# Optimization experiments

Hardware: AMD Instinct MI355X
Metric: run time of the kernel (lower is better)

The kernel has to match this reference:

```python
import jax, jax.numpy as jnp
import numpy as np

B, S, DIM = 1, 2048, 4096
NH, NKV, HD = 32, 8, 128
REPEATS = NH // NKV
ROPE_THETA = 10000.0


def setup_inputs() -> dict:
    key = jax.random.key(0)
    ks = jax.random.split(key, 6)
    x = jax.random.normal(ks[0], (B, S, DIM), jnp.float32) * 0.02
    wq = jax.random.normal(ks[1], (NH * HD, DIM), jnp.float32) * 0.02
    wk = jax.random.normal(ks[2], (NKV * HD, DIM), jnp.float32) * 0.02
    wv = jax.random.normal(ks[3], (NKV * HD, DIM), jnp.float32) * 0.02
    wo = jax.random.normal(ks[4], (DIM, NH * HD), jnp.float32) * 0.02
    # rotary frequencies (real cos/sin form of complex freqs_cis)
    inv_freq = 1.0 / (ROPE_THETA ** (jnp.arange(0, HD, 2, dtype=jnp.float32) / HD))
    ang = jnp.arange(S, dtype=jnp.float32)[:, None] * inv_freq[None, :]  # [S, HD//2]
    freqs_cos = jnp.cos(ang)
    freqs_sin = jnp.sin(ang)
    positions = jnp.arange(S, dtype=jnp.int32)  # prompt phase: all positions
    # additive causal mask
    mask = jnp.where(jnp.tril(jnp.ones((S, S), bool)), 0.0, -1e9).astype(jnp.float32)
    cache_k = jnp.zeros((B, S, NKV, HD), jnp.float32)
    cache_v = jnp.zeros((B, S, NKV, HD), jnp.float32)
    return dict(x=x, wq=wq, wk=wk, wv=wv, wo=wo, freqs_cos=freqs_cos,
                freqs_sin=freqs_sin, cache_k=cache_k, cache_v=cache_v,
                positions=positions, mask=mask)


def apply_rope(t, cos, sin):
    # t: [b, s, h, d]; pairs are (d0,d1),(d2,d3),... matching view_as_complex
    tr = t[..., 0::2]
    ti = t[..., 1::2]
    c = cos[None, :, None, :]
    s = sin[None, :, None, :]
    out_r = tr * c - ti * s
    out_i = tr * s + ti * c
    return jnp.stack([out_r, out_i], axis=-1).reshape(t.shape)


def reference(x, wq, wk, wv, wo, freqs_cos, freqs_sin, cache_k, cache_v, positions, mask):
    b, s, _ = x.shape
    xq = jnp.einsum('bsd,od->bso', x, wq).reshape(b, s, NH, HD)
    xk = jnp.einsum('bsd,od->bso', x, wk).reshape(b, s, NKV, HD)
    xv = jnp.einsum('bsd,od->bso', x, wv).reshape(b, s, NKV, HD)
    xq = apply_rope(xq, freqs_cos, freqs_sin)
    xk = apply_rope(xk, freqs_cos, freqs_sin)
    # KV-cache scatter (prompt phase writes; output uses fresh xk/xv here)
    cache_k = cache_k.at[:, positions].set(xk)
    cache_v = cache_v.at[:, positions].set(xv)
    # GQA: repeat_interleave kv heads to match query heads
    k = jnp.repeat(xk, REPEATS, axis=2).transpose(0, 2, 1, 3)  # [b, NH, s, HD]
    v = jnp.repeat(xv, REPEATS, axis=2).transpose(0, 2, 1, 3)
    q = xq.transpose(0, 2, 1, 3)
    scale = HD ** -0.5
    scores = jnp.einsum('bhqd,bhkd->bhqk', q, k) * scale + mask[None, None]
    probs = jax.nn.softmax(scores.astype(jnp.float32), axis=-1).astype(q.dtype)
    out = jnp.einsum('bhqk,bhkd->bhqd', probs, v)
    out = out.transpose(0, 2, 1, 3).reshape(b, s, NH * HD)
    return jnp.einsum('bso,do->bsd', out, wo)
```

## Files before the change

kernel.cpp:

```cpp
#include <hip/hip_runtime.h>
#include <hip/hip_bf16.h>
#include <stdint.h>

typedef __bf16 bf16_t;
typedef __attribute__((ext_vector_type(8))) __bf16 bf16x8;
typedef __attribute__((ext_vector_type(4))) float f32x4;
typedef __attribute__((ext_vector_type(8))) unsigned short u16x8;

#define S_LEN 2048
#define DIM   4096
#define QKVN  6144
#define NHEAD 32
#define HDIM  128

typedef __attribute__((address_space(1))) unsigned int as1_u32;
typedef __attribute__((address_space(3))) unsigned int as3_u32;

__device__ __forceinline__ unsigned short f2bf(float f) {
  unsigned u = __builtin_bit_cast(unsigned, f);
  u += 0x7fffu + ((u >> 16) & 1u);
  return (unsigned short)(u >> 16);
}

__device__ __forceinline__ void gload_lds16(const void* g, void* l) {
  __builtin_amdgcn_global_load_lds(
      (as1_u32*)(unsigned long long)(uintptr_t)g,
      (as3_u32*)(unsigned int)(uintptr_t)l,
      16, 0, 0);
}

__global__ __launch_bounds__(256) void cvt5_kernel(const float* __restrict__ x,
                                                   const float* __restrict__ wq,
                                                   const float* __restrict__ wk,
                                                   const float* __restrict__ wv,
                                                   const float* __restrict__ wo,
                                                   ushort4* __restrict__ xb,
                                                   ushort4* __restrict__ wqkvb,
                                                   ushort4* __restrict__ wob) {
  const long N0 = 2097152;
  const long N1 = N0 + 4194304;
  const long N2 = N1 + 1048576;
  const long N3 = N2 + 1048576;
  const long N4 = N3 + 4194304;
  long idx = (long)blockIdx.x * 256 + threadIdx.x;
  long stride = (long)gridDim.x * 256;
  for (long i = idx; i < N4; i += stride) {
    const float4* s; ushort4* d; long o;
    if (i < N0)      { s = (const float4*)x;  d = xb;              o = i; }
    else if (i < N1) { s = (const float4*)wq; d = wqkvb;           o = i - N0; }
    else if (i < N2) { s = (const float4*)wk; d = wqkvb + 4194304; o = i - N1; }
    else if (i < N3) { s = (const float4*)wv; d = wqkvb + 5242880; o = i - N2; }
    else             { s = (const float4*)wo; d = wob;             o = i - N3; }
    float4 v = s[o];
    ushort4 r;
    r.x = f2bf(v.x); r.y = f2bf(v.y); r.z = f2bf(v.z); r.w = f2bf(v.w);
    d[o] = r;
  }
}

__device__ __forceinline__ void stage_A(const bf16_t* __restrict__ g, int ldk,
                                        long rowBase, int k0, char* ldsBase, int tid) {
#pragma unroll
  for (int i = 0; i < 2; ++i) {
    int c = tid + i * 512;
    int row = c >> 2, slot = c & 3;
    const bf16_t* src = g + (rowBase + row) * (long)ldk + k0
                        + ((slot ^ ((row >> 1) & 3)) << 3);
    gload_lds16(src, ldsBase + c * 16);
  }
}

__device__ __forceinline__ void stage_B(const bf16_t* __restrict__ g, int ldk,
                                        long rowBase, int k0, char* ldsBase, int tid) {
  int row = tid >> 2, slot = tid & 3;
  const bf16_t* src = g + (rowBase + row) * (long)ldk + k0
                      + ((slot ^ ((row >> 1) & 3)) << 3);
  gload_lds16(src, ldsBase + tid * 16);
}

__device__ __forceinline__ bf16x8 frag_ld(const char* base, int row, int lg) {
  return *(const bf16x8*)(base + row * 64 + ((lg ^ ((row >> 1) & 3)) << 4));
}

template <int OUTF32>
__global__ __launch_bounds__(512, 2) void gemm256(const bf16_t* __restrict__ A,
                                                  const bf16_t* __restrict__ B,
                                                  void* __restrict__ Cout,
                                                  int M, int N, int K, int nxt) {
  __shared__ char lds[49152];
  const int tid = threadIdx.x;
  const int lane = tid & 63, w = tid >> 6;
  const int wm = w >> 1, wn = w & 1;
  const int lg = lane >> 4, lr = lane & 15;
  const int nwg = gridDim.x;
  const int orig = blockIdx.x;
  const int wgid = (orig & 7) * (nwg >> 3) + (orig >> 3);
  const int bx = wgid % nxt, by = wgid / nxt;
  const long rowA = (long)by * 256;
  const long rowB = (long)bx * 128;

  f32x4 acc[4][4];
  const f32x4 z4 = {0.f, 0.f, 0.f, 0.f};
#pragma unroll
  for (int i = 0; i < 4; ++i)
#pragma unroll
    for (int j = 0; j < 4; ++j) acc[i][j] = z4;

  stage_A(A, K, rowA, 0, lds, tid);
  stage_B(B, K, rowB, 0, lds + 16384, tid);
  stage_A(A, K, rowA, 32, lds + 24576, tid);
  stage_B(B, K, rowB, 32, lds + 40960, tid);
  asm volatile("s_waitcnt vmcnt(3)" ::: "memory");
  __builtin_amdgcn_s_barrier();

  const int nt = K >> 5;
  for (int t = 0; t < nt; ++t) {
    char* Ab = lds + (t & 1) * 24576;
    char* Bb = Ab + 16384;
    bf16x8 af[4], bfr[4];
#pragma unroll
    for (int mf = 0; mf < 4; ++mf) af[mf] = frag_ld(Ab, wm * 64 + mf * 16 + lr, lg);
#pragma unroll
    for (int nf = 0; nf < 4; ++nf) bfr[nf] = frag_ld(Bb, wn * 64 + nf * 16 + lr, lg);
    asm volatile("s_waitcnt lgkmcnt(0)" ::: "memory");
    __builtin_amdgcn_sched_barrier(0);
    __builtin_amdgcn_s_barrier();
    if (t + 2 < nt) {
      stage_A(A, K, rowA, (t + 2) * 32, Ab, tid);
      stage_B(B, K, rowB, (t + 2) * 32, Bb, tid);
    }
    __builtin_amdgcn_s_setprio(1);
#pragma unroll
    for (int mf = 0; mf < 4; ++mf)
#pragma unroll
      for (int nf = 0; nf < 4; ++nf)
        acc[mf][nf] = __builtin_amdgcn_mfma_f32_16x16x32_bf16(af[mf], bfr[nf],
                                                              acc[mf][nf], 0, 0, 0);
    __builtin_amdgcn_s_setprio(0);
    if (t + 2 < nt) {
      asm volatile("s_waitcnt vmcnt(3)" ::: "memory");
    } else {
      asm volatile("s_waitcnt vmcnt(0)" ::: "memory");
    }
    __builtin_amdgcn_s_barrier();
  }

  const long crow = rowA + wm * 64;
  const long ccol = rowB + wn * 64;
  if (OUTF32) {
    float* C = (float*)Cout;
#pragma unroll
    for (int mf = 0; mf < 4; ++mf)
#pragma unroll
      for (int j = 0; j < 4; ++j) {
        long row = crow + mf * 16 + lg * 4 + j;
        float* cp = C + row * N + ccol + lr;
#pragma unroll
        for (int nf = 0; nf < 4; ++nf) cp[nf * 16] = acc[mf][nf][j];
      }
  } else {
    unsigned short* C = (unsigned short*)Cout;
#pragma unroll
    for (int mf = 0; mf < 4; ++mf)
#pragma unroll
      for (int j = 0; j < 4; ++j) {
        long row = crow + mf * 16 + lg * 4 + j;
        unsigned short* cp = C + row * N + ccol + lr;
#pragma unroll
        for (int nf = 0; nf < 4; ++nf) cp[nf * 16] = f2bf(acc[mf][nf][j]);
      }
  }
}

__global__ __launch_bounds__(256) void rope_kernel(unsigned int* __restrict__ qkv32,
                                                   const float* __restrict__ cosb,
                                                   const float* __restrict__ sinb) {
  int t = blockIdx.x * 256 + threadIdx.x;
  int i  = t & 63;
  int sh = t >> 6;
  int hh = sh % 40;
  int s  = sh / 40;
  int col2 = (hh < 32) ? (hh * 64 + i) : (2048 + (hh - 32) * 64 + i);
  unsigned int* p = qkv32 + (long)s * (QKVN / 2) + col2;
  unsigned int v = *p;
  float tr = __builtin_bit_cast(float, (v & 0xffffu) << 16);
  float ti = __builtin_bit_cast(float, v & 0xffff0000u);
  float c  = cosb[s * 64 + i];
  float sn = sinb[s * 64 + i];
  float orr = tr * c - ti * sn;
  float oi  = tr * sn + ti * c;
  *p = (unsigned int)f2bf(orr) | ((unsigned int)f2bf(oi) << 16);
}

__global__ __launch_bounds__(256) void vtrans_kernel(const bf16_t* __restrict__ qkv,
                                                     bf16_t* __restrict__ vT) {
  const int kh = blockIdx.x;
  const int hd = threadIdx.x & 127;
  const int s0 = blockIdx.y * 16 + (threadIdx.x >> 7) * 8;
  u16x8 v;
#pragma unroll
  for (int e = 0; e < 8; ++e)
    v[e] = *(const unsigned short*)(qkv + (long)(s0 + e) * QKVN + 5120 + kh * HDIM + hd);
  *(u16x8*)(vT + ((long)kh * HDIM + hd) * S_LEN + s0) = v;
}

__global__ __launch_bounds__(512) void attn_kernel(const bf16_t* __restrict__ qkv,
                                                   const bf16_t* __restrict__ vT,
                                                   unsigned short* __restrict__ ob) {
  __shared__ bf16_t Kt[64 * 128];
  __shared__ bf16_t Vt[128 * 64];
  __shared__ bf16_t Pl[8 * 16 * 64];
  const int h  = blockIdx.x;
  const int qi = 15 - (int)blockIdx.y;
  const int qb = qi * 128;
  const int kh = h >> 2;
  const int tid = threadIdx.x, lane = tid & 63, w = tid >> 6;
  const int lg = lane >> 4, lr = lane & 15;
  const int qrow0 = qb + w * 16;

  bf16x8 qf[4];
  const bf16_t* qptr = qkv + (long)(qrow0 + lr) * QKVN + h * HDIM + lg * 8;
#pragma unroll
  for (int kk = 0; kk < 4; ++kk) qf[kk] = *(const bf16x8*)(qptr + kk * 32);

  const f32x4 z4 = {0.f, 0.f, 0.f, 0.f};
  f32x4 oacc[8];
#pragma unroll
  for (int c = 0; c < 8; ++c) oacc[c] = z4;
  float m[4]    = {-1e30f, -1e30f, -1e30f, -1e30f};
  float lsum[4] = {0.f, 0.f, 0.f, 0.f};

  char* KtB = (char*)Kt;
  char* VtB = (char*)Vt;
  char* PlB = (char*)Pl + w * 2048;
  const float scale = 0.08838834764831845f;
  const int ntiles = 2 * qi + 2;
  const int wqmax = qrow0 + 15;

  for (int t = 0; t < ntiles; ++t) {
    const int kv0 = t * 64;
    __syncthreads();
#pragma unroll
    for (int it = 0; it < 2; ++it) {
      int cch = tid + it * 512;
      int r = cch >> 4, c = cch & 15;
      const bf16_t* src = qkv + (long)(kv0 + r) * QKVN + 4096 + kh * HDIM
                          + ((c ^ (r & 7)) * 8);
      gload_lds16(src, KtB + cch * 16);
    }
#pragma unroll
    for (int it = 0; it < 2; ++it) {
      int cch = tid + it * 512;
      int hd = cch >> 3, c = cch & 7;
      const bf16_t* src = vT + ((long)kh * HDIM + hd) * S_LEN + kv0
                          + ((c ^ (hd & 7)) * 8);
      gload_lds16(src, VtB + cch * 16);
    }
    __syncthreads();
    if (kv0 > wqmax) continue;

    f32x4 sf[4];
#pragma unroll
    for (int f = 0; f < 4; ++f) {
      f32x4 a = z4;
      int n = f * 16 + lr;
      int rb = n * 256, sw = (n & 7) << 4;
#pragma unroll
      for (int kk = 0; kk < 4; ++kk) {
        bf16x8 kf = *(const bf16x8*)(KtB + rb + (((kk * 4 + lg) * 16) ^ sw));
        a = __builtin_amdgcn_mfma_f32_16x16x32_bf16(qf[kk], kf, a, 0, 0, 0);
      }
      sf[f] = a;
    }

    float sc_arr[4];
#pragma unroll
    for (int j = 0; j < 4; ++j) {
      int qrow = qrow0 + lg * 4 + j;
      float sv[4];
#pragma unroll
      for (int f = 0; f < 4; ++f) {
        float s = sf[f][j] * scale;
        if (kv0 + f * 16 + lr > qrow) s = -1e9f;
        sv[f] = s;
      }
      float mx = fmaxf(fmaxf(sv[0], sv[1]), fmaxf(sv[2], sv[3]));
      mx = fmaxf(mx, __shfl_xor(mx, 1));
      mx = fmaxf(mx, __shfl_xor(mx, 2));
      mx = fmaxf(mx, __shfl_xor(mx, 4));
      mx = fmaxf(mx, __shfl_xor(mx, 8));
      float mn = fmaxf(m[j], mx);
      float p[4];
#pragma unroll
      for (int f = 0; f < 4; ++f) p[f] = __expf(sv[f] - mn);
      float ps = (p[0] + p[1]) + (p[2] + p[3]);
      ps += __shfl_xor(ps, 1);
      ps += __shfl_xor(ps, 2);
      ps += __shfl_xor(ps, 4);
      ps += __shfl_xor(ps, 8);
      float sc = __expf(m[j] - mn);
      lsum[j] = lsum[j] * sc + ps;
      m[j] = mn;
      sc_arr[j] = sc;
      int row = lg * 4 + j;
      int swp = (row & 7) << 4;
#pragma unroll
      for (int f = 0; f < 4; ++f)
        *(unsigned short*)(PlB + row * 128 + (((f * 16 + lr) * 2) ^ swp)) = f2bf(p[f]);
    }
#pragma unroll
    for (int c = 0; c < 8; ++c)
#pragma unroll
      for (int j = 0; j < 4; ++j) oacc[c][j] *= sc_arr[j];

    bf16x8 pfr[2];
#pragma unroll
    for (int kk = 0; kk < 2; ++kk)
      pfr[kk] = *(const bf16x8*)(PlB + lr * 128 + (((kk * 4 + lg) * 16) ^ ((lr & 7) << 4)));
#pragma unroll
    for (int c = 0; c < 8; ++c) {
      int hd = c * 16 + lr;
      int rb = hd * 128, sw = (hd & 7) << 4;
#pragma unroll
      for (int kk = 0; kk < 2; ++kk) {
        bf16x8 vf = *(const bf16x8*)(VtB + rb + (((kk * 4 + lg) * 16) ^ sw));
        oacc[c] = __builtin_amdgcn_mfma_f32_16x16x32_bf16(pfr[kk], vf, oacc[c], 0, 0, 0);
      }
    }
  }

  float rl[4];
#pragma unroll
  for (int j = 0; j < 4; ++j) rl[j] = 1.f / lsum[j];
#pragma unroll
  for (int c = 0; c < 8; ++c)
#pragma unroll
    for (int j = 0; j < 4; ++j) {
      long row = qrow0 + lg * 4 + j;
      ob[row * 4096 + h * 128 + c * 16 + lr] = f2bf(oacc[c][j] * rl[j]);
    }
}

extern "C" void kernel_launch(void* const* d_in, const int* in_sizes, int n_in,
                              void* d_out, int out_size, void* d_ws, size_t ws_size,
                              hipStream_t stream) {
  const float* x  = (const float*)d_in[0];
  const float* wq = (const float*)d_in[1];
  const float* wk = (const float*)d_in[2];
  const float* wv = (const float*)d_in[3];
  const float* wo = (const float*)d_in[4];
  const float* fc = (const float*)d_in[5];
  const float* fs = (const float*)d_in[6];

  char* ws = (char*)d_ws;
  bf16_t* xb    = (bf16_t*)(ws + 0);
  bf16_t* wqkvb = (bf16_t*)(ws + 16777216);
  bf16_t* wob   = (bf16_t*)(ws + 67108864);
  bf16_t* qkv   = (bf16_t*)(ws + 100663296);
  bf16_t* ob    = (bf16_t*)(ws + 125829120);
  bf16_t* vT    = (bf16_t*)(ws + 0);

  cvt5_kernel<<<2048, 256, 0, stream>>>(x, wq, wk, wv, wo,
                                        (ushort4*)xb, (ushort4*)wqkvb, (ushort4*)wob);

  gemm256<0><<<384, 512, 0, stream>>>(xb, wqkvb, qkv, 2048, 6144, 4096, 48);
  vtrans_kernel<<<dim3(8, 128), 256, 0, stream>>>(qkv, vT);
  rope_kernel<<<20480, 256, 0, stream>>>((unsigned int*)qkv, fc, fs);
  attn_kernel<<<dim3(32, 16), 512, 0, stream>>>(qkv, vT, (unsigned short*)ob);
  gemm256<1><<<256, 512, 0, stream>>>(ob, wob, d_out, 2048, 4096, 4096, 32);
}
```

Baseline: 354.4 us.

## Enlarge GEMM tiles to 256x256 with K=64 and a phased LDS pipeline

Replaces the 256x128, K=32 GEMM with a 256x256-tile kernel that uses 64-wide K steps. It double-buffers 128KB of LDS with an XOR swizzle over 128-byte rows. Each iteration is split into four MFMA phases, and the A and B half-tile loads for later steps are spread between them. The aim is more data reuse per loaded byte and better overlap of global-to-LDS copies with MFMA work. In exchange, the grid shrinks to 192 and 128 workgroups, which on a 256-CU part may leave many CUs idle. The large LDS footprint also limits occupancy to one block per CU.

```diff
diff --git a/kernel.cpp b/kernel.cpp
--- a/kernel.cpp
+++ b/kernel.cpp
@@ -58,99 +58,144 @@
   }
 }
 
-__device__ __forceinline__ void stage_A(const bf16_t* __restrict__ g, int ldk,
-                                        long rowBase, int k0, char* ldsBase, int tid) {
-#pragma unroll
-  for (int i = 0; i < 2; ++i) {
-    int c = tid + i * 512;
-    int row = c >> 2, slot = c & 3;
-    const bf16_t* src = g + (rowBase + row) * (long)ldk + k0
-                        + ((slot ^ ((row >> 1) & 3)) << 3);
-    gload_lds16(src, ldsBase + c * 16);
-  }
-}
-
-__device__ __forceinline__ void stage_B(const bf16_t* __restrict__ g, int ldk,
-                                        long rowBase, int k0, char* ldsBase, int tid) {
-  int row = tid >> 2, slot = tid & 3;
-  const bf16_t* src = g + (rowBase + row) * (long)ldk + k0
-                      + ((slot ^ ((row >> 1) & 3)) << 3);
-  gload_lds16(src, ldsBase + tid * 16);
-}
-
-__device__ __forceinline__ bf16x8 frag_ld(const char* base, int row, int lg) {
-  return *(const bf16x8*)(base + row * 64 + ((lg ^ ((row >> 1) & 3)) << 4));
+__device__ __forceinline__ bf16x8 fld(const char* half, int row, int chunk) {
+  return *(const bf16x8*)(half + row * 128 + ((chunk ^ (row & 7)) << 4));
+}
+
+__device__ __forceinline__ void mfma8(const bf16x8 (*af)[2], const bf16x8 (*bf_)[2],
+                                      f32x4 (*acc)[4], int mbase, int nbase) {
+#pragma unroll
+  for (int m = 0; m < 4; ++m)
+#pragma unroll
+    for (int n = 0; n < 2; ++n) {
+      acc[mbase + m][nbase + n] = __builtin_amdgcn_mfma_f32_16x16x32_bf16(
+          af[mbase + m][0], bf_[nbase + n][0], acc[mbase + m][nbase + n], 0, 0, 0);
+      acc[mbase + m][nbase + n] = __builtin_amdgcn_mfma_f32_16x16x32_bf16(
+          af[mbase + m][1], bf_[nbase + n][1], acc[mbase + m][nbase + n], 0, 0, 0);
+    }
 }
 
 template <int OUTF32>
-__global__ __launch_bounds__(512, 2) void gemm256(const bf16_t* __restrict__ A,
-                                                  const bf16_t* __restrict__ B,
-                                                  void* __restrict__ Cout,
-                                                  int M, int N, int K, int nxt) {
-  __shared__ char lds[49152];
+__global__ __launch_bounds__(512, 2) void gemm8p(const bf16_t* __restrict__ A,
+                                                 const bf16_t* __restrict__ B,
+                                                 void* __restrict__ Cout,
+                                                 int M, int N, int K, int nxt) {
+  __shared__ char lds[131072];
   const int tid = threadIdx.x;
   const int lane = tid & 63, w = tid >> 6;
-  const int wm = w >> 1, wn = w & 1;
+  const int wm = w >> 2, wn = w & 3;
   const int lg = lane >> 4, lr = lane & 15;
   const int nwg = gridDim.x;
   const int orig = blockIdx.x;
   const int wgid = (orig & 7) * (nwg >> 3) + (orig >> 3);
   const int bx = wgid % nxt, by = wgid / nxt;
   const long rowA = (long)by * 256;
-  const long rowB = (long)bx * 128;
-
-  f32x4 acc[4][4];
+  const long rowB = (long)bx * 256;
+
+  f32x4 acc[8][4];
   const f32x4 z4 = {0.f, 0.f, 0.f, 0.f};
 #pragma unroll
-  for (int i = 0; i < 4; ++i)
+  for (int i = 0; i < 8; ++i)
 #pragma unroll
     for (int j = 0; j < 4; ++j) acc[i][j] = z4;
 
-  stage_A(A, K, rowA, 0, lds, tid);
-  stage_B(B, K, rowB, 0, lds + 16384, tid);
-  stage_A(A, K, rowA, 32, lds + 24576, tid);
-  stage_B(B, K, rowB, 32, lds + 40960, tid);
-  asm volatile("s_waitcnt vmcnt(3)" ::: "memory");
+  const int r0 = tid >> 3, sl = tid & 7;
+  const long xo  = (long)((sl ^ (r0 & 7)) << 3);
+  const long aof = (rowA + r0) * (long)K + xo;
+  const long bof = (rowB + r0) * (long)K + xo;
+  const long j1  = (long)64 * K;
+  const long h1  = (long)128 * K;
+  const int ld0 = tid * 16, ld1 = (tid + 512) * 16;
+
+#define STG_A(K0, HALF, DBUF)                                                  \
+  { char* hp = lds + (DBUF) * 65536 + (HALF) * 16384;                          \
+    gload_lds16(A + aof + (HALF) * h1 + (K0),      hp + ld0);                  \
+    gload_lds16(A + aof + (HALF) * h1 + j1 + (K0), hp + ld1); }
+#define STG_B(K0, HALF, DBUF)                                                  \
+  { char* hp = lds + (DBUF) * 65536 + 32768 + (HALF) * 16384;                  \
+    gload_lds16(B + bof + (HALF) * h1 + (K0),      hp + ld0);                  \
+    gload_lds16(B + bof + (HALF) * h1 + j1 + (K0), hp + ld1); }
+
+  const int nt = K >> 6;
+  const int bro = (wn & 1) * 64;
+
+  STG_A(0, 0, 0); STG_A(0, 1, 0); STG_B(0, 0, 0); STG_B(0, 1, 0);
+  STG_B(64, 0, 1); STG_B(64, 1, 1);
+  asm volatile("s_waitcnt vmcnt(4)" ::: "memory");
   __builtin_amdgcn_s_barrier();
 
-  const int nt = K >> 5;
+  bf16x8 af[8][2], bf_[4][2];
+
   for (int t = 0; t < nt; ++t) {
-    char* Ab = lds + (t & 1) * 24576;
-    char* Bb = Ab + 16384;
-    bf16x8 af[4], bfr[4];
-#pragma unroll
-    for (int mf = 0; mf < 4; ++mf) af[mf] = frag_ld(Ab, wm * 64 + mf * 16 + lr, lg);
-#pragma unroll
-    for (int nf = 0; nf < 4; ++nf) bfr[nf] = frag_ld(Bb, wn * 64 + nf * 16 + lr, lg);
+    const int d = t & 1;
+    const char* Ah = lds + d * 65536 + wm * 16384;
+    const char* Bh = lds + d * 65536 + 32768 + (wn >> 1) * 16384;
+    const int k1 = (t + 1) << 6, k2 = (t + 2) << 6;
+#pragma unroll
+    for (int m = 0; m < 4; ++m) {
+      af[m][0] = fld(Ah, m * 16 + lr, lg);
+      af[m][1] = fld(Ah, m * 16 + lr, 4 + lg);
+    }
+#pragma unroll
+    for (int n = 0; n < 2; ++n) {
+      bf_[n][0] = fld(Bh, bro + n * 16 + lr, lg);
+      bf_[n][1] = fld(Bh, bro + n * 16 + lr, 4 + lg);
+    }
+    if (t + 1 < nt) STG_A(k1, 0, d ^ 1);
+    __builtin_amdgcn_s_barrier();
     asm volatile("s_waitcnt lgkmcnt(0)" ::: "memory");
     __builtin_amdgcn_sched_barrier(0);
-    __builtin_amdgcn_s_barrier();
-    if (t + 2 < nt) {
-      stage_A(A, K, rowA, (t + 2) * 32, Ab, tid);
-      stage_B(B, K, rowB, (t + 2) * 32, Bb, tid);
-    }
     __builtin_amdgcn_s_setprio(1);
-#pragma unroll
-    for (int mf = 0; mf < 4; ++mf)
-#pragma unroll
-      for (int nf = 0; nf < 4; ++nf)
-        acc[mf][nf] = __builtin_amdgcn_mfma_f32_16x16x32_bf16(af[mf], bfr[nf],
-                                                              acc[mf][nf], 0, 0, 0);
+    mfma8(af, bf_, acc, 0, 0);
+    __builtin_amdgcn_s_setprio(0);
+    __builtin_amdgcn_s_barrier();
+#pragma unroll
+    for (int n = 2; n < 4; ++n) {
+      bf_[n][0] = fld(Bh, bro + n * 16 + lr, lg);
+      bf_[n][1] = fld(Bh, bro + n * 16 + lr, 4 + lg);
+    }
+    if (t + 1 < nt) STG_A(k1, 1, d ^ 1);
+    __builtin_amdgcn_s_barrier();
+    asm volatile("s_waitcnt lgkmcnt(0)" ::: "memory");
+    __builtin_amdgcn_sched_barrier(0);
+    __builtin_amdgcn_s_setprio(1);
+    mfma8(af, bf_, acc, 0, 2);
+    __builtin_amdgcn_s_setprio(0);
+    __builtin_amdgcn_s_barrier();
+#pragma unroll
+    for (int m = 4; m < 8; ++m) {
+      af[m][0] = fld(Ah, m * 16 + lr, lg);
+      af[m][1] = fld(Ah, m * 16 + lr, 4 + lg);
+    }
+    if (t + 2 < nt) STG_B(k2, 0, d);
+    __builtin_amdgcn_s_barrier();
+    asm volatile("s_waitcnt lgkmcnt(0)" ::: "memory");
+    __builtin_amdgcn_sched_barrier(0);
+    __builtin_amdgcn_s_setprio(1);
+    mfma8(af, bf_, acc, 4, 0);
+    __builtin_amdgcn_s_setprio(0);
+    __builtin_amdgcn_s_barrier();
+    if (t + 2 < nt) STG_B(k2, 1, d);
+    __builtin_amdgcn_s_barrier();
+    __builtin_amdgcn_s_setprio(1);
+    mfma8(af, bf_, acc, 4, 2);
     __builtin_amdgcn_s_setprio(0);
     if (t + 2 < nt) {
-      asm volatile("s_waitcnt vmcnt(3)" ::: "memory");
+      asm volatile("s_waitcnt vmcnt(4)" ::: "memory");
     } else {
       asm volatile("s_waitcnt vmcnt(0)" ::: "memory");
     }
     __builtin_amdgcn_s_barrier();
   }
-
-  const long crow = rowA + wm * 64;
+#undef STG_A
+#undef STG_B
+
+  const long crow = rowA + wm * 128;
   const long ccol = rowB + wn * 64;
   if (OUTF32) {
     float* C = (float*)Cout;
 #pragma unroll
-    for (int mf = 0; mf < 4; ++mf)
+    for (int mf = 0; mf < 8; ++mf)
 #pragma unroll
       for (int j = 0; j < 4; ++j) {
         long row = crow + mf * 16 + lg * 4 + j;
@@ -161,7 +206,7 @@
   } else {
     unsigned short* C = (unsigned short*)Cout;
 #pragma unroll
-    for (int mf = 0; mf < 4; ++mf)
+    for (int mf = 0; mf < 8; ++mf)
 #pragma unroll
       for (int j = 0; j < 4; ++j) {
         long row = crow + mf * 16 + lg * 4 + j;
@@ -363,9 +408,9 @@
   cvt5_kernel<<<2048, 256, 0, stream>>>(x, wq, wk, wv, wo,
                                         (ushort4*)xb, (ushort4*)wqkvb, (ushort4*)wob);
 
-  gemm256<0><<<384, 512, 0, stream>>>(xb, wqkvb, qkv, 2048, 6144, 4096, 48);
+  gemm8p<0><<<192, 512, 0, stream>>>(xb, wqkvb, qkv, 2048, 6144, 4096, 24);
   vtrans_kernel<<<dim3(8, 128), 256, 0, stream>>>(qkv, vT);
   rope_kernel<<<20480, 256, 0, stream>>>((unsigned int*)qkv, fc, fs);
   attn_kernel<<<dim3(32, 16), 512, 0, stream>>>(qkv, vT, (unsigned short*)ob);
-  gemm256<1><<<256, 512, 0, stream>>>(ob, wob, d_out, 2048, 4096, 4096, 32);
-}
+  gemm8p<1><<<128, 512, 0, stream>>>(ob, wob, d_out, 2048, 4096, 4096, 16);
+}
```

After: 359.7 us. About the same (+1.5%).
